# Kernel optimization log

Hardware: AMD Instinct MI355X
Metric: run time of the kernel (lower is better)

Reference implementation:

```python
import jax, jax.numpy as jnp
import numpy as np

B, S, D = 4, 2048, 2048   # batch, seq, hidden
E, F, K = 8, 1024, 2      # experts, expert ffn dim, top-k
SF = 1024                 # shared-expert ffn dim
EPS = 1e-6


def setup_inputs() -> dict:
    key = jax.random.key(0)
    ks = jax.random.split(key, 9)
    g = lambda k, shape, scale: (jax.random.normal(k, shape, jnp.float32) * scale)
    return {
        "x": g(ks[0], (B, S, D), 1.0),
        "rms_weight": jnp.ones((D,), jnp.float32),
        "router_w": g(ks[1], (D, E), 0.02),
        "w_gate": g(ks[2], (E, D, F), 0.02),
        "w_up": g(ks[3], (E, D, F), 0.02),
        "w_down": g(ks[4], (E, F, D), 0.02),
        "sw_gate": g(ks[5], (D, SF), 0.02),
        "sw_up": g(ks[6], (D, SF), 0.02),
        "sw_down": g(ks[7], (SF, D), 0.02),
    }


def _rmsnorm(x, w, eps=EPS):
    var = jnp.mean(x * x, axis=-1, keepdims=True)
    return x * jax.lax.rsqrt(var + eps) * w


def reference(x, rms_weight, router_w, w_gate, w_up, w_down, sw_gate, sw_up, sw_down):
    b, s, d = x.shape
    e = router_w.shape[1]
    h = _rmsnorm(x, rms_weight)
    ht = h.reshape(-1, d)                      # [T, D] tokens
    t = ht.shape[0]

    # Router: softmax over experts, top-k, renormalize selected weights
    logits = ht @ router_w                     # [T, E]
    probs = jax.nn.softmax(logits, axis=-1)
    topv, topi = jax.lax.top_k(probs, K)       # [T, K]
    topv = topv / jnp.sum(topv, axis=-1, keepdims=True)
    # dense [T, E] combine weights (zero for non-selected experts)
    w_dense = jnp.zeros((t, e), ht.dtype).at[jnp.arange(t)[:, None], topi].set(topv)

    # Expert SwiGLU MLPs (grouped GEMM expressed densely over experts)
    g = jnp.einsum('td,edf->tef', ht, w_gate)  # [T, E, F]
    u = jnp.einsum('td,edf->tef', ht, w_up)
    eo = jnp.einsum('tef,efd->ted', jax.nn.silu(g) * u, w_down)  # [T, E, D]
    moe = jnp.einsum('te,ted->td', w_dense, eo)                   # weighted combine

    # Shared expert (SwiGLU)
    sh = (jax.nn.silu(ht @ sw_gate) * (ht @ sw_up)) @ sw_down

    return (moe + sh).reshape(b, s, d)
```

## Files before the change

kernel.cpp:

```cpp
#include <hip/hip_runtime.h>
#include <stdint.h>

#define T_TOK 8192
#define DDIM  2048
#define NEXP  8
#define FDIM  1024
#define CAP   25600
#define NT_M  200
#define BK    64
#define GXT   16
#define NBLK  (GXT * NT_M)
#define CPX   (NBLK / 8)
#define NTJ   27648

typedef __bf16 bf16x8 __attribute__((ext_vector_type(8)));
typedef float  f32x4  __attribute__((ext_vector_type(4)));

typedef const __attribute__((address_space(1))) uint32_t* as1_u32;
typedef __attribute__((address_space(3))) uint32_t* as3_u32;

__device__ __forceinline__ void gload16(const void* g, void* l) {
  __builtin_amdgcn_global_load_lds((as1_u32)g, (as3_u32)l, 16, 0, 0);
}
__device__ __forceinline__ float bf2f(uint16_t u) {
  union { uint32_t i; float f; } v; v.i = ((uint32_t)u) << 16; return v.f;
}
__device__ __forceinline__ uint16_t f2bf(float f) {
  union { float f; uint32_t i; } v; v.f = f;
  uint32_t i = v.i;
  i += 0x7FFFu + ((i >> 16) & 1u);
  return (uint16_t)(i >> 16);
}
__device__ __forceinline__ void mk_offs(const int* __restrict__ counts, int* o) {
  int a = 0;
  #pragma unroll
  for (int e = 0; e < NEXP; e++) { o[e] = a; a += (counts[e] + 127) & ~127; }
  o[8] = a; o[9] = a + T_TOK;
}

__global__ __launch_bounds__(256) void k_prep(
    const float* __restrict__ wg, const float* __restrict__ wu,
    const float* __restrict__ sg, const float* __restrict__ su,
    const float* __restrict__ wd, const float* __restrict__ sd,
    const float* __restrict__ x, const float* __restrict__ rmsw,
    const float* __restrict__ router_w,
    uint16_t* __restrict__ wgT, uint16_t* __restrict__ wuT,
    uint16_t* __restrict__ sgT, uint16_t* __restrict__ suT,
    uint16_t* __restrict__ wdT, uint16_t* __restrict__ sdT,
    uint16_t* __restrict__ h, int* __restrict__ topi,
    float* __restrict__ topw, int* __restrict__ counts)
{
  int flat = blockIdx.x;
  if (flat < NTJ) {
    const float* src; uint16_t* dst;
    int Csrc, Rdst, r0, c0;
    if (flat < 18432) {
      int z = flat >> 10, rem = flat & 1023;
      Csrc = FDIM; Rdst = DDIM;
      r0 = (rem >> 4) << 5;
      c0 = (rem & 15) << 6;
      if (z < 8)       { src = wg + (size_t)z * DDIM * FDIM;       dst = wgT + (size_t)z * FDIM * DDIM; }
      else if (z < 16) { src = wu + (size_t)(z - 8) * DDIM * FDIM; dst = wuT + (size_t)(z - 8) * FDIM * DDIM; }
      else if (z == 16){ src = sg; dst = sgT; }
      else             { src = su; dst = suT; }
    } else {
      int f2 = flat - 18432;
      int z = f2 >> 10, rem = f2 & 1023;
      Csrc = DDIM; Rdst = FDIM;
      r0 = (rem >> 5) << 5;
      c0 = (rem & 31) << 6;
      if (z < 8) { src = wd + (size_t)z * FDIM * DDIM; dst = wdT + (size_t)z * DDIM * FDIM; }
      else       { src = sd; dst = sdT; }
    }
    int lane = threadIdx.x & 63, w = threadIdx.x >> 6;
    int c = c0 + lane;
    int rbase = r0 + w * 8;
    const float* sp = src + (size_t)rbase * Csrc + c;
    float v[8];
    #pragma unroll
    for (int j = 0; j < 8; j++) v[j] = sp[(size_t)j * Csrc];
    uint4 o;
    o.x = (uint32_t)f2bf(v[0]) | ((uint32_t)f2bf(v[1]) << 16);
    o.y = (uint32_t)f2bf(v[2]) | ((uint32_t)f2bf(v[3]) << 16);
    o.z = (uint32_t)f2bf(v[4]) | ((uint32_t)f2bf(v[5]) << 16);
    o.w = (uint32_t)f2bf(v[6]) | ((uint32_t)f2bf(v[7]) << 16);
    *(uint4*)(dst + (size_t)c * Rdst + rbase) = o;
  } else {
    int wv = threadIdx.x >> 6, lane = threadIdx.x & 63;
    int t = (flat - NTJ) * 4 + wv;
    const float* xr = x + (size_t)t * DDIM;

    float4 xv[8], wv8[8];
    #pragma unroll
    for (int j = 0; j < 8; j++) {
      xv[j]  = ((const float4*)xr)[j * 64 + lane];
      wv8[j] = ((const float4*)rmsw)[j * 64 + lane];
    }
    float ss = 0.f;
    #pragma unroll
    for (int j = 0; j < 8; j++)
      ss += xv[j].x * xv[j].x + xv[j].y * xv[j].y + xv[j].z * xv[j].z + xv[j].w * xv[j].w;
    #pragma unroll
    for (int m = 32; m >= 1; m >>= 1) ss += __shfl_xor(ss, m, 64);
    float scale = rsqrtf(ss * (1.0f / DDIM) + 1e-6f);

    float hv[8][4];
    #pragma unroll
    for (int j = 0; j < 8; j++) {
      hv[j][0] = xv[j].x * scale * wv8[j].x;
      hv[j][1] = xv[j].y * scale * wv8[j].y;
      hv[j][2] = xv[j].z * scale * wv8[j].z;
      hv[j][3] = xv[j].w * scale * wv8[j].w;
      ushort4 hw;
      hw.x = f2bf(hv[j][0]); hw.y = f2bf(hv[j][1]);
      hw.z = f2bf(hv[j][2]); hw.w = f2bf(hv[j][3]);
      ((ushort4*)(h + (size_t)t * DDIM))[j * 64 + lane] = hw;
    }

    float lp[8] = {0, 0, 0, 0, 0, 0, 0, 0};
    #pragma unroll
    for (int j = 0; j < 8; j++) {
      #pragma unroll
      for (int c = 0; c < 4; c++) {
        int d = (j * 64 + lane) * 4 + c;
        const float* rw = router_w + (size_t)d * NEXP;
        float4 a = ((const float4*)rw)[0];
        float4 b = ((const float4*)rw)[1];
        float hj = hv[j][c];
        lp[0] += hj * a.x; lp[1] += hj * a.y; lp[2] += hj * a.z; lp[3] += hj * a.w;
        lp[4] += hj * b.x; lp[5] += hj * b.y; lp[6] += hj * b.z; lp[7] += hj * b.w;
      }
    }
    #pragma unroll
    for (int m = 32; m >= 1; m >>= 1) {
      #pragma unroll
      for (int e = 0; e < 8; e++) lp[e] += __shfl_xor(lp[e], m, 64);
    }
    if (lane == 0) {
      int i0 = 0;
      for (int e = 1; e < 8; e++) if (lp[e] > lp[i0]) i0 = e;
      int i1 = (i0 == 0) ? 1 : 0;
      for (int e = 0; e < 8; e++) if (e != i0 && lp[e] > lp[i1]) i1 = e;
      float p0 = 1.f / (1.f + expf(lp[i1] - lp[i0]));
      topi[t * 2] = i0; topi[t * 2 + 1] = i1;
      topw[t * 2] = p0; topw[t * 2 + 1] = 1.f - p0;
      atomicAdd(&counts[i0], 1);
      atomicAdd(&counts[i1], 1);
    }
  }
}

__global__ __launch_bounds__(256) void k_scatter(
    const int* __restrict__ topi, const float* __restrict__ topw,
    const int* __restrict__ counts, int* __restrict__ cursor,
    int* __restrict__ tokslot, float* __restrict__ wtrow)
{
  int offs[10];
  mk_offs(counts, offs);
  int idx = blockIdx.x * 256 + threadIdx.x;
  if (idx < T_TOK * 2) {
    int t = idx >> 1, k = idx & 1;
    int e = topi[idx];
    int slot = atomicAdd(&cursor[e], 1);
    int row = offs[e] + slot;
    tokslot[row] = t * 4 + k;
    wtrow[row] = topw[idx];
  } else {
    int t = idx - T_TOK * 2;
    int row = offs[8] + t;
    tokslot[row] = t * 4 + 2;
    wtrow[row] = 1.0f;
  }
}

#define BUFA(c) (ldsu + (size_t)(c) * 16384)
#define BUFB(c) (ldsu + 8192 + (size_t)(c) * 16384)

#define XCD_REMAP()                                                            \
  int flat_ = blockIdx.y * GXT + blockIdx.x;                                   \
  int nf_ = (flat_ & 7) * CPX + (flat_ >> 3);                                  \
  int bx = nf_ & (GXT - 1);                                                    \
  int by = nf_ / GXT;

#define STAGE8(T, C) do {                                                     \
  _Pragma("unroll") for (int i_ = 0; i_ < 4; i_++) {                          \
    int G_ = w * 256 + i_ * 64 + lane;                                        \
    gload16(aSrc[i_] + (size_t)(T) * BK, BUFA(C) + G_ * 8);                   \
    gload16(bSrc[i_] + (size_t)(T) * BK, BUFB(C) + G_ * 8);                   \
  } } while (0)

#define COMPUTE_TILE(curA, curB) do {                                         \
  _Pragma("unroll") for (int ks_ = 0; ks_ < 2; ks_++) {                       \
    int ce_ = ks_ * 32 + ((lane >> 4) << 3);                                  \
    bf16x8 av_[4], bv_[4];                                                    \
    _Pragma("unroll") for (int m_ = 0; m_ < 4; m_++) {                        \
      int rr_ = wr * 64 + m_ * 16 + (lane & 15);                              \
      av_[m_] = *(const bf16x8*)((curA) + rr_ * 64 + (ce_ ^ ((rr_ & 7) << 3))); \
    }                                                                         \
    _Pragma("unroll") for (int n_ = 0; n_ < 4; n_++) {                        \
      int rr_ = wc * 64 + n_ * 16 + (lane & 15);                              \
      bv_[n_] = *(const bf16x8*)((curB) + rr_ * 64 + (ce_ ^ ((rr_ & 7) << 3))); \
    }                                                                         \
    __builtin_amdgcn_s_setprio(1);                                            \
    _Pragma("unroll") for (int m_ = 0; m_ < 4; m_++)                          \
    _Pragma("unroll") for (int n_ = 0; n_ < 4; n_++)                          \
      acc[m_][n_] = __builtin_amdgcn_mfma_f32_16x16x32_bf16(av_[m_], bv_[n_], acc[m_][n_], 0, 0, 0); \
    __builtin_amdgcn_s_setprio(0);                                            \
  } } while (0)

__global__ __launch_bounds__(256, 2) void k_stage1(
    const uint16_t* __restrict__ h, const uint16_t* __restrict__ wgT,
    const uint16_t* __restrict__ wuT, const uint16_t* __restrict__ sgT,
    const uint16_t* __restrict__ suT, const int* __restrict__ counts,
    const int* __restrict__ tokslot, uint16_t* __restrict__ A_int)
{
  __shared__ __align__(16) uint16_t ldsu[32768];

  int offs[10];
  mk_offs(counts, offs);
  XCD_REMAP();
  int row0 = by * 128;
  int end = offs[9];
  if (row0 >= end) return;
  int e = 0;
  #pragma unroll 1
  for (; e < 9; e++) if (row0 >= offs[e] && row0 < offs[e + 1]) break;
  const uint16_t* bg = (e < NEXP) ? wgT + (size_t)e * FDIM * DDIM : sgT;
  const uint16_t* bu = (e < NEXP) ? wuT + (size_t)e * FDIM * DDIM : suT;
  int f0 = bx * 64;

  int tid = threadIdx.x, lane = tid & 63, w = tid >> 6;
  int wr = w & 1, wc = w >> 1;

  const uint16_t* aSrc[4];
  const uint16_t* bSrc[4];
  #pragma unroll
  for (int i = 0; i < 4; i++) {
    int G = w * 256 + i * 64 + lane;
    int r = G >> 3, sl = G & 7;
    int gl = sl ^ (r & 7);
    int ts = tokslot[row0 + r];
    int tok = ts < 0 ? 0 : (ts >> 2);
    aSrc[i] = h + (size_t)tok * DDIM + gl * 8;
    int b = r >> 4;
    int fc = f0 + ((b >> 1) << 4) + (r & 15);
    const uint16_t* wbase = (b & 1) ? bu : bg;
    bSrc[i] = wbase + (size_t)fc * DDIM + gl * 8;
  }

  f32x4 acc[4][4] = {};
  const int NT = DDIM / BK;

  STAGE8(0, 0);
  __syncthreads();

  #pragma unroll 1
  for (int t = 0; t < NT; ++t) {
    int cur = t & 1;
    if (t + 1 < NT) STAGE8(t + 1, cur ^ 1);
    const uint16_t* curA = BUFA(cur);
    const uint16_t* curB = BUFB(cur);
    COMPUTE_TILE(curA, curB);
    __syncthreads();
  }

  #pragma unroll
  for (int m = 0; m < 4; m++) {
    #pragma unroll
    for (int p = 0; p < 2; p++) {
      #pragma unroll
      for (int r = 0; r < 4; r++) {
        int row = row0 + wr * 64 + m * 16 + ((lane >> 4) << 2) + r;
        int col = f0 + wc * 32 + p * 16 + (lane & 15);
        float g = acc[m][2 * p][r];
        float u = acc[m][2 * p + 1][r];
        float a = (g / (1.f + expf(-g))) * u;
        A_int[(size_t)row * FDIM + col] = f2bf(a);
      }
    }
  }
}

__global__ __launch_bounds__(256, 2) void k_stage2(
    const uint16_t* __restrict__ A_int, const uint16_t* __restrict__ wdT,
    const uint16_t* __restrict__ sdT, const int* __restrict__ counts,
    const int* __restrict__ tokslot, const float* __restrict__ wtrow,
    uint16_t* __restrict__ eo, float* __restrict__ out)
{
  __shared__ __align__(16) uint16_t ldsu[32768];

  int offs[10];
  mk_offs(counts, offs);
  XCD_REMAP();
  int row0 = by * 128;
  int end = offs[9];
  if (row0 >= end) return;
  int e = 0;
  #pragma unroll 1
  for (; e < 9; e++) if (row0 >= offs[e] && row0 < offs[e + 1]) break;
  const uint16_t* bw = (e < NEXP) ? wdT + (size_t)e * DDIM * FDIM : sdT;
  int d0 = bx * 128;

  int tid = threadIdx.x, lane = tid & 63, w = tid >> 6;
  int wr = w & 1, wc = w >> 1;

  const uint16_t* aSrc[4];
  const uint16_t* bSrc[4];
  #pragma unroll
  for (int i = 0; i < 4; i++) {
    int G = w * 256 + i * 64 + lane;
    int r = G >> 3, sl = G & 7;
    int gl = sl ^ (r & 7);
    aSrc[i] = A_int + (size_t)(row0 + r) * FDIM + gl * 8;
    bSrc[i] = bw + (size_t)(d0 + r) * FDIM + gl * 8;
  }

  f32x4 acc[4][4] = {};
  const int NT = FDIM / BK;

  STAGE8(0, 0);
  __syncthreads();

  #pragma unroll 1
  for (int t = 0; t < NT; ++t) {
    int cur = t & 1;
    if (t + 1 < NT) STAGE8(t + 1, cur ^ 1);
    const uint16_t* curA = BUFA(cur);
    const uint16_t* curB = BUFB(cur);
    COMPUTE_TILE(curA, curB);
    __syncthreads();
  }

  #pragma unroll
  for (int m = 0; m < 4; m++) {
    #pragma unroll
    for (int r = 0; r < 4; r++) {
      int grow = row0 + wr * 64 + m * 16 + ((lane >> 4) << 2) + r;
      int ts = tokslot[grow];
      if (ts < 0) continue;
      int tok = ts >> 2, slot = ts & 3;
      if (slot == 2) {
        size_t obase = (size_t)tok * DDIM;
        #pragma unroll
        for (int n = 0; n < 4; n++) {
          int col = d0 + wc * 64 + n * 16 + (lane & 15);
          out[obase + col] = acc[m][n][r];
        }
      } else {
        float wt = wtrow[grow];
        size_t obase = ((size_t)tok * 2 + slot) * DDIM;
        #pragma unroll
        for (int n = 0; n < 4; n++) {
          int col = d0 + wc * 64 + n * 16 + (lane & 15);
          eo[obase + col] = f2bf(acc[m][n][r] * wt);
        }
      }
    }
  }
}

__global__ __launch_bounds__(256) void k_final(
    const uint16_t* __restrict__ eo, float* __restrict__ out)
{
  int tok = blockIdx.x;
  int col = threadIdx.x * 8;
  const uint16_t* e0 = eo + ((size_t)tok * 2) * DDIM + col;
  const uint16_t* e1 = eo + ((size_t)tok * 2 + 1) * DDIM + col;
  float* op = out + (size_t)tok * DDIM + col;
  ushort4 a0 = *(const ushort4*)(e0);
  ushort4 a1 = *(const ushort4*)(e0 + 4);
  ushort4 b0 = *(const ushort4*)(e1);
  ushort4 b1 = *(const ushort4*)(e1 + 4);
  float4 s0 = *(const float4*)(op);
  float4 s1 = *(const float4*)(op + 4);
  float4 o0, o1;
  o0.x = s0.x + bf2f(a0.x) + bf2f(b0.x);
  o0.y = s0.y + bf2f(a0.y) + bf2f(b0.y);
  o0.z = s0.z + bf2f(a0.z) + bf2f(b0.z);
  o0.w = s0.w + bf2f(a0.w) + bf2f(b0.w);
  o1.x = s1.x + bf2f(a1.x) + bf2f(b1.x);
  o1.y = s1.y + bf2f(a1.y) + bf2f(b1.y);
  o1.z = s1.z + bf2f(a1.z) + bf2f(b1.z);
  o1.w = s1.w + bf2f(a1.w) + bf2f(b1.w);
  *(float4*)(op) = o0;
  *(float4*)(op + 4) = o1;
}

extern "C" void kernel_launch(void* const* d_in, const int* in_sizes, int n_in,
                              void* d_out, int out_size, void* d_ws, size_t ws_size,
                              hipStream_t stream) {
  (void)in_sizes; (void)n_in; (void)out_size;
  const float* x    = (const float*)d_in[0];
  const float* rmsw = (const float*)d_in[1];
  const float* rtw  = (const float*)d_in[2];
  const float* wg   = (const float*)d_in[3];
  const float* wu   = (const float*)d_in[4];
  const float* wd   = (const float*)d_in[5];
  const float* sg   = (const float*)d_in[6];
  const float* su   = (const float*)d_in[7];
  const float* sd   = (const float*)d_in[8];
  float* out = (float*)d_out;

  char* base = (char*)d_ws;
  size_t off_b = 0;
  auto place = [&](size_t bytes) { size_t r = off_b; off_b += (bytes + 255) & ~(size_t)255; return r; };
  size_t o_topi    = place((size_t)T_TOK * 2 * 4);
  size_t o_topw    = place((size_t)T_TOK * 2 * 4);
  size_t o_counts  = place(64);
  size_t o_cursor  = place(64);
  size_t o_tokslot = place((size_t)CAP * 4);
  size_t o_wtrow   = place((size_t)CAP * 4);
  size_t o_h   = place((size_t)T_TOK * DDIM * 2);
  size_t o_wgT = place((size_t)NEXP * FDIM * DDIM * 2);
  size_t o_wuT = place((size_t)NEXP * FDIM * DDIM * 2);
  size_t o_sgT = place((size_t)FDIM * DDIM * 2);
  size_t o_suT = place((size_t)FDIM * DDIM * 2);
  size_t o_wdT = place((size_t)NEXP * DDIM * FDIM * 2);
  size_t o_sdT = place((size_t)DDIM * FDIM * 2);
  size_t o_Ai  = place((size_t)CAP * FDIM * 2);
  size_t o_eo  = o_h;
  size_t NEED = off_b;
  if (ws_size < NEED) return;

  int*      topi    = (int*)(base + o_topi);
  float*    topw    = (float*)(base + o_topw);
  int*      counts  = (int*)(base + o_counts);
  int*      cursor  = (int*)(base + o_cursor);
  int*      tokslot = (int*)(base + o_tokslot);
  float*    wtrow   = (float*)(base + o_wtrow);
  uint16_t* h       = (uint16_t*)(base + o_h);
  uint16_t* wgT     = (uint16_t*)(base + o_wgT);
  uint16_t* wuT     = (uint16_t*)(base + o_wuT);
  uint16_t* sgT     = (uint16_t*)(base + o_sgT);
  uint16_t* suT     = (uint16_t*)(base + o_suT);
  uint16_t* wdT     = (uint16_t*)(base + o_wdT);
  uint16_t* sdT     = (uint16_t*)(base + o_sdT);
  uint16_t* Ai      = (uint16_t*)(base + o_Ai);
  uint16_t* eo      = (uint16_t*)(base + o_eo);

  hipMemsetAsync(counts, 0, 512, stream);
  hipMemsetAsync(tokslot, 0xFF, (size_t)CAP * 4, stream);

  k_prep<<<NTJ + T_TOK / 4, 256, 0, stream>>>(
      wg, wu, sg, su, wd, sd, x, rmsw, rtw,
      wgT, wuT, sgT, suT, wdT, sdT, h, topi, topw, counts);

  k_scatter<<<(T_TOK * 3) / 256, 256, 0, stream>>>(topi, topw, counts, cursor, tokslot, wtrow);

  k_stage1<<<dim3(GXT, NT_M), 256, 0, stream>>>(h, wgT, wuT, sgT, suT, counts, tokslot, Ai);
  k_stage2<<<dim3(GXT, NT_M), 256, 0, stream>>>(Ai, wdT, sdT, counts, tokslot, wtrow, eo, out);
  k_final<<<T_TOK, 256, 0, stream>>>(eo, out);
}
```

Before: 732.5 us.

## Transpose weights through swizzled LDS tiles with coalesced float4 loads and 16-byte stores

The weight transpose-and-convert step in the prep kernel now processes 256x128 tiles per block. Each block loads rows with float4 coalesced reads, writes bf16 into an XOR-swizzled LDS buffer, and writes transposed rows out as 16-byte chunks. This replaces many small blocks that did strided scalar loads, so global memory traffic for the roughly 150MB weight conversion should be better coalesced. The cost is 64KB of static LDS per block, which also applies to the RMSNorm/router blocks in the same kernel and lowers their occupancy.

```diff
diff --git a/kernel.cpp b/kernel.cpp
--- a/kernel.cpp
+++ b/kernel.cpp
@@ -11,7 +11,7 @@
 #define GXT   16
 #define NBLK  (GXT * NT_M)
 #define CPX   (NBLK / 8)
-#define NTJ   27648
+#define NRG   1728
 
 typedef __bf16 bf16x8 __attribute__((ext_vector_type(8)));
 typedef float  f32x4  __attribute__((ext_vector_type(4)));
@@ -37,6 +37,8 @@
   for (int e = 0; e < NEXP; e++) { o[e] = a; a += (counts[e] + 127) & ~127; }
   o[8] = a; o[9] = a + T_TOK;
 }
+
+#define SWZ(c) ((((c) >> 2) & 15) << 3)
 
 __global__ __launch_bounds__(256) void k_prep(
     const float* __restrict__ wg, const float* __restrict__ wu,
@@ -50,45 +52,54 @@
     uint16_t* __restrict__ h, int* __restrict__ topi,
     float* __restrict__ topw, int* __restrict__ counts)
 {
+  __shared__ uint16_t lds[128 * 256];
   int flat = blockIdx.x;
-  if (flat < NTJ) {
+  int t = threadIdx.x;
+  if (flat < NRG) {
     const float* src; uint16_t* dst;
     int Csrc, Rdst, r0, c0;
-    if (flat < 18432) {
-      int z = flat >> 10, rem = flat & 1023;
+    if (flat < 1152) {
+      int z = flat >> 6, rem = flat & 63;
       Csrc = FDIM; Rdst = DDIM;
-      r0 = (rem >> 4) << 5;
-      c0 = (rem & 15) << 6;
+      r0 = (rem >> 3) << 8;
+      c0 = (rem & 7) << 7;
       if (z < 8)       { src = wg + (size_t)z * DDIM * FDIM;       dst = wgT + (size_t)z * FDIM * DDIM; }
       else if (z < 16) { src = wu + (size_t)(z - 8) * DDIM * FDIM; dst = wuT + (size_t)(z - 8) * FDIM * DDIM; }
       else if (z == 16){ src = sg; dst = sgT; }
       else             { src = su; dst = suT; }
     } else {
-      int f2 = flat - 18432;
-      int z = f2 >> 10, rem = f2 & 1023;
+      int f2 = flat - 1152;
+      int z = f2 >> 6, rem = f2 & 63;
       Csrc = DDIM; Rdst = FDIM;
-      r0 = (rem >> 5) << 5;
-      c0 = (rem & 31) << 6;
+      r0 = (rem >> 4) << 8;
+      c0 = (rem & 15) << 7;
       if (z < 8) { src = wd + (size_t)z * FDIM * DDIM; dst = wdT + (size_t)z * DDIM * FDIM; }
       else       { src = sd; dst = sdT; }
     }
-    int lane = threadIdx.x & 63, w = threadIdx.x >> 6;
-    int c = c0 + lane;
-    int rbase = r0 + w * 8;
-    const float* sp = src + (size_t)rbase * Csrc + c;
-    float v[8];
-    #pragma unroll
-    for (int j = 0; j < 8; j++) v[j] = sp[(size_t)j * Csrc];
-    uint4 o;
-    o.x = (uint32_t)f2bf(v[0]) | ((uint32_t)f2bf(v[1]) << 16);
-    o.y = (uint32_t)f2bf(v[2]) | ((uint32_t)f2bf(v[3]) << 16);
-    o.z = (uint32_t)f2bf(v[4]) | ((uint32_t)f2bf(v[5]) << 16);
-    o.w = (uint32_t)f2bf(v[6]) | ((uint32_t)f2bf(v[7]) << 16);
-    *(uint4*)(dst + (size_t)c * Rdst + rbase) = o;
+    int sub = t >> 5;
+    int cq = (t & 31) * 4;
+    #pragma unroll 4
+    for (int it = 0; it < 32; it++) {
+      int r = it * 8 + sub;
+      float4 v = *(const float4*)(src + (size_t)(r0 + r) * Csrc + c0 + cq);
+      lds[(cq + 0) * 256 + (r ^ SWZ(cq + 0))] = f2bf(v.x);
+      lds[(cq + 1) * 256 + (r ^ SWZ(cq + 1))] = f2bf(v.y);
+      lds[(cq + 2) * 256 + (r ^ SWZ(cq + 2))] = f2bf(v.z);
+      lds[(cq + 3) * 256 + (r ^ SWZ(cq + 3))] = f2bf(v.w);
+    }
+    __syncthreads();
+    #pragma unroll 4
+    for (int it = 0; it < 16; it++) {
+      int chunk = it * 256 + t;
+      int cl = chunk >> 5;
+      int rch = (chunk & 31) * 8;
+      uint4 o = *(const uint4*)(lds + cl * 256 + (rch ^ SWZ(cl)));
+      *(uint4*)(dst + (size_t)(c0 + cl) * Rdst + r0 + rch) = o;
+    }
   } else {
-    int wv = threadIdx.x >> 6, lane = threadIdx.x & 63;
-    int t = (flat - NTJ) * 4 + wv;
-    const float* xr = x + (size_t)t * DDIM;
+    int wv = t >> 6, lane = t & 63;
+    int tok = (flat - NRG) * 4 + wv;
+    const float* xr = x + (size_t)tok * DDIM;
 
     float4 xv[8], wv8[8];
     #pragma unroll
@@ -114,7 +125,7 @@
       ushort4 hw;
       hw.x = f2bf(hv[j][0]); hw.y = f2bf(hv[j][1]);
       hw.z = f2bf(hv[j][2]); hw.w = f2bf(hv[j][3]);
-      ((ushort4*)(h + (size_t)t * DDIM))[j * 64 + lane] = hw;
+      ((ushort4*)(h + (size_t)tok * DDIM))[j * 64 + lane] = hw;
     }
 
     float lp[8] = {0, 0, 0, 0, 0, 0, 0, 0};
@@ -142,8 +153,8 @@
       int i1 = (i0 == 0) ? 1 : 0;
       for (int e = 0; e < 8; e++) if (e != i0 && lp[e] > lp[i1]) i1 = e;
       float p0 = 1.f / (1.f + expf(lp[i1] - lp[i0]));
-      topi[t * 2] = i0; topi[t * 2 + 1] = i1;
-      topw[t * 2] = p0; topw[t * 2 + 1] = 1.f - p0;
+      topi[tok * 2] = i0; topi[tok * 2 + 1] = i1;
+      topw[tok * 2] = p0; topw[tok * 2 + 1] = 1.f - p0;
       atomicAdd(&counts[i0], 1);
       atomicAdd(&counts[i1], 1);
     }
@@ -441,7 +452,7 @@
   hipMemsetAsync(counts, 0, 512, stream);
   hipMemsetAsync(tokslot, 0xFF, (size_t)CAP * 4, stream);
 
-  k_prep<<<NTJ + T_TOK / 4, 256, 0, stream>>>(
+  k_prep<<<NRG + T_TOK / 4, 256, 0, stream>>>(
       wg, wu, sg, su, wd, sd, x, rmsw, rtw,
       wgT, wuT, sgT, suT, wdT, sdT, h, topi, topw, counts);
 
```

New measurement: 717.8 us (median of 2 runs). -2.0%, faster.
